# Kernel tuning notes

Measured on AMD Instinct MI355X. Metric: run time of the kernel, lower is better.

Reference implementation:

```python
import jax, jax.numpy as jnp
import numpy as np

B, S, D = 4, 2048, 1024
E, H, K = 32, 128, 2


def setup_inputs() -> dict:
    key = jax.random.key(0)
    k1, k2, k3, k4 = jax.random.split(key, 4)
    scale_d = 1.0 / np.sqrt(D)
    scale_h = 1.0 / np.sqrt(H)
    return {
        "x": jax.random.normal(k1, (B, S, D), dtype=jnp.float32),
        "w_sel": jax.random.normal(k2, (E, D), dtype=jnp.float32) * scale_d,      # router Linear weight [E, D]
        "w_keys": jax.random.normal(k3, (E, D, H), dtype=jnp.float32) * scale_d,  # per-expert up-proj
        "w_values": jax.random.normal(k4, (E, H, D), dtype=jnp.float32) * scale_h, # per-expert down-proj
        "k": K,
    }


def reference(x, w_sel, w_keys, w_values, k):
    # Router: sigmoid gating + top-k expert selection per token.
    sel = jax.nn.sigmoid(jnp.einsum('bsd,ed->bse', x, w_sel))      # [B,S,E]
    sel_val, sel_idx = jax.lax.top_k(sel, k)                       # [B,S,k]
    n_exp = w_sel.shape[0]
    # Dense gate matrix: gate[b,s,e] = sum of sel_val over heads routed to e
    # (top_k indices are distinct, so this matches the per-head accumulation).
    gate = jnp.sum(jax.nn.one_hot(sel_idx, n_exp, dtype=x.dtype) * sel_val[..., None], axis=-2)  # [B,S,E]
    # Expert up-projection + ReLU for all experts (dense equivalent of the
    # per-token gathered keys[expert_idx](token); unselected experts are
    # zeroed by the gate so the math is identical).
    scores = jax.nn.relu(jnp.einsum('bsd,edh->bseh', x, w_keys))   # [B,S,E,H]
    weighted = scores * gate[..., None]                            # [B,S,E,H]
    out = jnp.einsum('bseh,ehd->bsd', weighted, w_values)          # [B,S,D]
    return out
```

## Files before the change

kernel.cpp:

```cpp
#include <hip/hip_runtime.h>
#include <cstdint>
#include <cstddef>

#define NTOK 8192
#define DIM  1024
#define NEXP 32
#define NH   128
#define TT   64
#define FTILES 16
#define BK   128
#define RT   32
#define LCAP 1024

typedef __attribute__((ext_vector_type(8))) short short8;
typedef __attribute__((ext_vector_type(4))) float float4_;

static __device__ __forceinline__ unsigned short f2bf(float f) {
  unsigned u = __float_as_uint(f);
  return (unsigned short)((u + 0x7fffu + ((u >> 16) & 1u)) >> 16);
}
static __device__ __forceinline__ float bf2f(unsigned short h) {
  return __uint_as_float(((unsigned)h) << 16);
}
static __device__ __forceinline__ void gload_lds16(const unsigned short* g,
                                                   unsigned short* l) {
  __builtin_amdgcn_global_load_lds(
      (const __attribute__((address_space(1))) unsigned int*)(const void*)g,
      (__attribute__((address_space(3))) unsigned int*)(void*)l, 16, 0, 0);
}

__global__ __launch_bounds__(256) void prep_kernel(
    const float* __restrict__ w_keys, const float* __restrict__ w_values,
    const float* __restrict__ x,
    unsigned short* __restrict__ wk_t, unsigned short* __restrict__ wv_t,
    unsigned short* __restrict__ xbf, int* __restrict__ counts)
{
  __shared__ float tile[32][33];
  const int bid = blockIdx.x;
  const int tid = threadIdx.x;
  if (bid == 0 && tid < NEXP) counts[tid] = 0;

  if (bid < 8192) {
    const float* src; unsigned short* dst; int R, C, lb;
    if (bid < 4096) { src = w_keys;   dst = wk_t; R = DIM; C = NH;  lb = bid; }
    else            { src = w_values; dst = wv_t; R = NH;  C = DIM; lb = bid - 4096; }
    const int e  = lb >> 7;
    const int t  = lb & 127;
    const int tpc = C >> 5;
    const int r0 = (t / tpc) * 32;
    const int c0 = (t % tpc) * 32;
    const float* s = src + (size_t)e * R * C;
    unsigned short* d = dst + (size_t)e * R * C;

    const int i = tid >> 3;
    const int j = (tid & 7) * 4;
    float4 v = *(const float4*)(s + (size_t)(r0 + i) * C + c0 + j);
    tile[i][j] = v.x; tile[i][j + 1] = v.y; tile[i][j + 2] = v.z; tile[i][j + 3] = v.w;
    __syncthreads();
    unsigned lo = (unsigned)f2bf(tile[j + 0][i]) | ((unsigned)f2bf(tile[j + 1][i]) << 16);
    unsigned hi = (unsigned)f2bf(tile[j + 2][i]) | ((unsigned)f2bf(tile[j + 3][i]) << 16);
    uint2 u; u.x = lo; u.y = hi;
    *(uint2*)(d + (size_t)(c0 + i) * R + r0 + j) = u;
  } else {
    const int lb = bid - 8192;
    size_t i = ((size_t)lb * 256 + tid) * 8;
    float4 a = *(const float4*)(x + i);
    float4 b = *(const float4*)(x + i + 4);
    uint4 u;
    u.x = (unsigned)f2bf(a.x) | ((unsigned)f2bf(a.y) << 16);
    u.y = (unsigned)f2bf(a.z) | ((unsigned)f2bf(a.w) << 16);
    u.z = (unsigned)f2bf(b.x) | ((unsigned)f2bf(b.y) << 16);
    u.w = (unsigned)f2bf(b.z) | ((unsigned)f2bf(b.w) << 16);
    *(uint4*)(xbf + i) = u;
  }
}

__global__ __launch_bounds__(256) void router_kernel(
    const float* __restrict__ x, const float* __restrict__ w_sel,
    int* __restrict__ counts, unsigned* __restrict__ list)
{
  __shared__ __align__(16) float xs_t[64][36];
  __shared__ float ws[NEXP][65];
  __shared__ float S[RT][33];

  const int tid  = threadIdx.x;
  const int tok0 = blockIdx.x * RT;
  const int tr   = tid >> 3;
  const int d8   = (tid & 7) * 8;
  const int tg4  = (tid & 7) * 4;

  float acc[4] = {0.f, 0.f, 0.f, 0.f};

  for (int dc = 0; dc < DIM; dc += 64) {
    const float* xp = x + (size_t)(tok0 + tr) * DIM + dc + d8;
    float4 a0 = *(const float4*)(xp);
    float4 a1 = *(const float4*)(xp + 4);
    xs_t[d8 + 0][tr] = a0.x; xs_t[d8 + 1][tr] = a0.y;
    xs_t[d8 + 2][tr] = a0.z; xs_t[d8 + 3][tr] = a0.w;
    xs_t[d8 + 4][tr] = a1.x; xs_t[d8 + 5][tr] = a1.y;
    xs_t[d8 + 6][tr] = a1.z; xs_t[d8 + 7][tr] = a1.w;
    const float* wp = w_sel + (size_t)tr * DIM + dc + d8;
    float4 b0 = *(const float4*)(wp);
    float4 b1 = *(const float4*)(wp + 4);
    ws[tr][d8 + 0] = b0.x; ws[tr][d8 + 1] = b0.y;
    ws[tr][d8 + 2] = b0.z; ws[tr][d8 + 3] = b0.w;
    ws[tr][d8 + 4] = b1.x; ws[tr][d8 + 5] = b1.y;
    ws[tr][d8 + 6] = b1.z; ws[tr][d8 + 7] = b1.w;
    __syncthreads();

    #pragma unroll 8
    for (int d = 0; d < 64; ++d) {
      float w = ws[tr][d];
      float4 xv = *(const float4*)&xs_t[d][tg4];
      acc[0] += xv.x * w; acc[1] += xv.y * w;
      acc[2] += xv.z * w; acc[3] += xv.w * w;
    }
    __syncthreads();
  }

  #pragma unroll
  for (int j = 0; j < 4; ++j)
    S[tg4 + j][tr] = acc[j];
  __syncthreads();

  if (tid < RT) {
    const int t = tid;
    float m1 = -1e30f, m2 = -1e30f;
    int i1 = 0, i2 = 0;
    for (int ee = 0; ee < NEXP; ++ee) {
      float v = S[t][ee];
      if (v > m1)      { m2 = m1; i2 = i1; m1 = v; i1 = ee; }
      else if (v > m2) { m2 = v; i2 = ee; }
    }
    const int token = tok0 + t;
    float g1 = 1.f / (1.f + __expf(-m1));
    float g2 = 1.f / (1.f + __expf(-m2));
    unsigned e1 = ((unsigned)f2bf(g1) << 16) | ((unsigned)token << 1);
    unsigned e2 = ((unsigned)f2bf(g2) << 16) | ((unsigned)token << 1) | 1u;
    int p1 = atomicAdd(&counts[i1], 1);
    if (p1 < LCAP) list[i1 * LCAP + p1] = e1;
    int p2 = atomicAdd(&counts[i2], 1);
    if (p2 < LCAP) list[i2 * LCAP + p2] = e2;
  }
}

__global__ __launch_bounds__(256, 2) void ffn_kernel(
    const unsigned short* __restrict__ xbf,
    const unsigned short* __restrict__ wk_t,
    const unsigned short* __restrict__ wv_t,
    float* __restrict__ out,
    unsigned short* __restrict__ cont,
    const int* __restrict__ counts, const unsigned* __restrict__ list,
    int use_cont)
{
  const int bid = blockIdx.x;
  const int e   = bid & 31;
  const int cnt = min(counts[e], LCAP);

  __shared__ unsigned short xsf[2][16 * 512];
  __shared__ unsigned short ss[TT][NH + 8];
  __shared__ int   toks[TT];
  __shared__ float gates[TT];

  const int tid  = threadIdx.x;
  const int wave = tid >> 6;
  const int lane = tid & 63;
  const int quad = lane >> 4;
  const int l16  = lane & 15;

  const unsigned short* wkb = wk_t + (size_t)e * NH * DIM;
  const unsigned short* wvb = wv_t + (size_t)e * DIM * NH;

  for (int t0 = (bid >> 5) * TT; t0 < cnt; t0 += FTILES * TT) {
    const int n_tok = min(TT, cnt - t0);

    if (tid < TT) {
      int valid = tid < n_tok;
      unsigned en = valid ? list[e * LCAP + t0 + tid] : 0u;
      toks[tid]  = valid ? (int)(en & 0xffffu) : -1;
      gates[tid] = valid ? bf2f((unsigned short)(en >> 16)) : 0.f;
    }
    __syncthreads();

    int slot = toks[wave * 16 + l16];
    int gtok = (slot < 0) ? 0 : (slot >> 1);
    const unsigned short* gsrc = xbf + (size_t)gtok * DIM + quad * 8;

    #pragma unroll
    for (int kk = 0; kk < 4; ++kk)
      gload_lds16(gsrc + kk * 32, &xsf[0][(wave * 4 + kk) * 512]);
    __syncthreads();

    float4_ acc[4][2];
    #pragma unroll
    for (int mt = 0; mt < 4; ++mt)
      #pragma unroll
      for (int nt = 0; nt < 2; ++nt) acc[mt][nt] = (float4_){0.f, 0.f, 0.f, 0.f};

    for (int ci = 0; ci < 8; ++ci) {
      const int dc = ci * BK;
      if (ci < 7) {
        const int nb = (ci + 1) & 1;
        #pragma unroll
        for (int kk = 0; kk < 4; ++kk)
          gload_lds16(gsrc + dc + BK + kk * 32, &xsf[nb][(wave * 4 + kk) * 512]);
      }
      short8 b[4][2];
      #pragma unroll
      for (int kk = 0; kk < 4; ++kk)
        #pragma unroll
        for (int nt = 0; nt < 2; ++nt)
          b[kk][nt] = *(const short8*)(wkb +
              (size_t)(wave * 32 + nt * 16 + l16) * DIM + dc + kk * 32 + quad * 8);

      const unsigned short* xb = &xsf[ci & 1][0];
      #pragma unroll
      for (int kk = 0; kk < 4; ++kk) {
        #pragma unroll
        for (int mt = 0; mt < 4; ++mt) {
          short8 a = *(const short8*)(xb + (mt * 4 + kk) * 512 + lane * 8);
          #pragma unroll
          for (int nt = 0; nt < 2; ++nt)
            acc[mt][nt] = __builtin_amdgcn_mfma_f32_16x16x32_bf16(a, b[kk][nt], acc[mt][nt], 0, 0, 0);
        }
      }
      __syncthreads();
    }

    #pragma unroll
    for (int mt = 0; mt < 4; ++mt)
      #pragma unroll
      for (int nt = 0; nt < 2; ++nt)
        #pragma unroll
        for (int r = 0; r < 4; ++r) {
          int row = mt * 16 + quad * 4 + r;
          float v = fmaxf(acc[mt][nt][r], 0.f) * gates[row];
          ss[row][wave * 32 + nt * 16 + l16] = f2bf(v);
        }
    __syncthreads();

    #pragma unroll 1
    for (int nc = 0; nc < 4; ++nc) {
      const int colbase = wave * 256 + nc * 64;
      float4_ o[4][4];
      #pragma unroll
      for (int mt = 0; mt < 4; ++mt)
        #pragma unroll
        for (int nt = 0; nt < 4; ++nt) o[mt][nt] = (float4_){0.f, 0.f, 0.f, 0.f};

      short8 b2[4][4];
      #pragma unroll
      for (int kk = 0; kk < 4; ++kk)
        #pragma unroll
        for (int nt = 0; nt < 4; ++nt)
          b2[kk][nt] = *(const short8*)(wvb +
              (size_t)(colbase + nt * 16 + l16) * NH + kk * 32 + quad * 8);

      #pragma unroll
      for (int kk = 0; kk < 4; ++kk) {
        short8 a[4];
        #pragma unroll
        for (int mt = 0; mt < 4; ++mt)
          a[mt] = *(const short8*)&ss[mt * 16 + l16][kk * 32 + quad * 8];
        #pragma unroll
        for (int mt = 0; mt < 4; ++mt)
          #pragma unroll
          for (int nt = 0; nt < 4; ++nt)
            o[mt][nt] = __builtin_amdgcn_mfma_f32_16x16x32_bf16(a[mt], b2[kk][nt], o[mt][nt], 0, 0, 0);
      }

      if (use_cont) {
        #pragma unroll
        for (int mt = 0; mt < 4; ++mt)
          #pragma unroll
          for (int r = 0; r < 4; ++r) {
            int row = mt * 16 + quad * 4 + r;
            if (row < n_tok) {
              int sl = toks[row];
              size_t base = ((size_t)((sl & 1) * NTOK + (sl >> 1))) * DIM + colbase;
              #pragma unroll
              for (int nt = 0; nt < 4; ++nt)
                cont[base + nt * 16 + l16] = f2bf(o[mt][nt][r]);
            }
          }
      } else {
        #pragma unroll
        for (int mt = 0; mt < 4; ++mt)
          #pragma unroll
          for (int r = 0; r < 4; ++r) {
            int row = mt * 16 + quad * 4 + r;
            if (row < n_tok) {
              size_t base = (size_t)(toks[row] >> 1) * DIM + colbase;
              #pragma unroll
              for (int nt = 0; nt < 4; ++nt)
                unsafeAtomicAdd(&out[base + nt * 16 + l16], o[mt][nt][r]);
            }
          }
      }
    }
    __syncthreads();
  }
}

__global__ __launch_bounds__(256) void combine_kernel(
    const unsigned short* __restrict__ cont, float* __restrict__ out)
{
  size_t i = ((size_t)blockIdx.x * 256 + threadIdx.x) * 8;
  uint4 a = *(const uint4*)(cont + i);
  uint4 b = *(const uint4*)(cont + (size_t)NTOK * DIM + i);
  float4 r0, r1;
  r0.x = bf2f((unsigned short)(a.x & 0xffff)) + bf2f((unsigned short)(b.x & 0xffff));
  r0.y = bf2f((unsigned short)(a.x >> 16))    + bf2f((unsigned short)(b.x >> 16));
  r0.z = bf2f((unsigned short)(a.y & 0xffff)) + bf2f((unsigned short)(b.y & 0xffff));
  r0.w = bf2f((unsigned short)(a.y >> 16))    + bf2f((unsigned short)(b.y >> 16));
  r1.x = bf2f((unsigned short)(a.z & 0xffff)) + bf2f((unsigned short)(b.z & 0xffff));
  r1.y = bf2f((unsigned short)(a.z >> 16))    + bf2f((unsigned short)(b.z >> 16));
  r1.z = bf2f((unsigned short)(a.w & 0xffff)) + bf2f((unsigned short)(b.w & 0xffff));
  r1.w = bf2f((unsigned short)(a.w >> 16))    + bf2f((unsigned short)(b.w >> 16));
  *(float4*)(out + i) = r0;
  *(float4*)(out + i + 4) = r1;
}

extern "C" void kernel_launch(void* const* d_in, const int* in_sizes, int n_in,
                              void* d_out, int out_size, void* d_ws, size_t ws_size,
                              hipStream_t stream) {
  (void)in_sizes; (void)n_in;
  const float* x        = (const float*)d_in[0];
  const float* w_sel    = (const float*)d_in[1];
  const float* w_keys   = (const float*)d_in[2];
  const float* w_values = (const float*)d_in[3];
  float* out = (float*)d_out;

  char* ws = (char*)d_ws;
  size_t off = 0;
  int*            counts = (int*)(ws + off);            off += 4096;
  unsigned*       list   = (unsigned*)(ws + off);       off += (size_t)NEXP * LCAP * 4;
  unsigned short* wk_t   = (unsigned short*)(ws + off); off += (size_t)NEXP * NH * DIM * 2;
  unsigned short* wv_t   = (unsigned short*)(ws + off); off += (size_t)NEXP * NH * DIM * 2;
  unsigned short* xbf    = (unsigned short*)(ws + off); off += (size_t)NTOK * DIM * 2;
  unsigned short* cont   = (unsigned short*)(ws + off);
  size_t need_full = off + (size_t)2 * NTOK * DIM * 2;
  const int use_cont = (ws_size >= need_full) ? 1 : 0;

  prep_kernel<<<12288, 256, 0, stream>>>(w_keys, w_values, x, wk_t, wv_t, xbf, counts);

  router_kernel<<<NTOK / RT, 256, 0, stream>>>(x, w_sel, counts, list);

  if (!use_cont)
    hipMemsetAsync(out, 0, (size_t)out_size * sizeof(float), stream);

  ffn_kernel<<<NEXP * FTILES, 256, 0, stream>>>(xbf, wk_t, wv_t, out, cont,
                                                counts, list, use_cont);

  if (use_cont)
    combine_kernel<<<NTOK * DIM / (256 * 8), 256, 0, stream>>>(cont, out);
}
```

Measured before the change: 249.8 us.

## Fuse x bf16 conversion into FFN, split routing lists per choice, flatten tile grid

The FFN kernel now reads fp32 x directly and converts it to bf16 while staging each tile, so the separate x conversion pass and its bf16 buffer go away. Routing lists are kept per (expert, choice), and blocks are mapped onto a flattened tile list rather than a fixed per-expert grid. First-choice results are written in fp32 straight to the output, and second-choice results go to a bf16 buffer, so the combine kernel reads a single bf16 buffer and adds it into the output. The router is rewritten as direct per-thread dot products without LDS tiling, the FFN prefetches weights into registers, and the counts are cleared with a small memset. The fixed grid of 320 blocks and a per-list cap of 512 can silently drop tokens if routing is very skewed.

```diff
diff --git a/kernel.cpp b/kernel.cpp
--- a/kernel.cpp
+++ b/kernel.cpp
@@ -1,4 +1,5 @@
 #include <hip/hip_runtime.h>
+#include <hip/hip_bf16.h>
 #include <cstdint>
 #include <cstddef>
 
@@ -7,10 +8,10 @@
 #define NEXP 32
 #define NH   128
 #define TT   64
-#define FTILES 16
 #define BK   128
-#define RT   32
-#define LCAP 1024
+#define LCAP2 512
+#define RTOK 16
+#define FGRID 320
 
 typedef __attribute__((ext_vector_type(8))) short short8;
 typedef __attribute__((ext_vector_type(4))) float float4_;
@@ -22,283 +23,296 @@
 static __device__ __forceinline__ float bf2f(unsigned short h) {
   return __uint_as_float(((unsigned)h) << 16);
 }
-static __device__ __forceinline__ void gload_lds16(const unsigned short* g,
-                                                   unsigned short* l) {
-  __builtin_amdgcn_global_load_lds(
-      (const __attribute__((address_space(1))) unsigned int*)(const void*)g,
-      (__attribute__((address_space(3))) unsigned int*)(void*)l, 16, 0, 0);
-}
-
-__global__ __launch_bounds__(256) void prep_kernel(
+
+__global__ __launch_bounds__(256) void transpose_cvt_kernel(
     const float* __restrict__ w_keys, const float* __restrict__ w_values,
-    const float* __restrict__ x,
-    unsigned short* __restrict__ wk_t, unsigned short* __restrict__ wv_t,
-    unsigned short* __restrict__ xbf, int* __restrict__ counts)
+    unsigned short* __restrict__ wk_t, unsigned short* __restrict__ wv_t)
 {
   __shared__ float tile[32][33];
   const int bid = blockIdx.x;
   const int tid = threadIdx.x;
-  if (bid == 0 && tid < NEXP) counts[tid] = 0;
-
-  if (bid < 8192) {
-    const float* src; unsigned short* dst; int R, C, lb;
-    if (bid < 4096) { src = w_keys;   dst = wk_t; R = DIM; C = NH;  lb = bid; }
-    else            { src = w_values; dst = wv_t; R = NH;  C = DIM; lb = bid - 4096; }
-    const int e  = lb >> 7;
-    const int t  = lb & 127;
-    const int tpc = C >> 5;
-    const int r0 = (t / tpc) * 32;
-    const int c0 = (t % tpc) * 32;
-    const float* s = src + (size_t)e * R * C;
-    unsigned short* d = dst + (size_t)e * R * C;
-
-    const int i = tid >> 3;
-    const int j = (tid & 7) * 4;
-    float4 v = *(const float4*)(s + (size_t)(r0 + i) * C + c0 + j);
-    tile[i][j] = v.x; tile[i][j + 1] = v.y; tile[i][j + 2] = v.z; tile[i][j + 3] = v.w;
-    __syncthreads();
-    unsigned lo = (unsigned)f2bf(tile[j + 0][i]) | ((unsigned)f2bf(tile[j + 1][i]) << 16);
-    unsigned hi = (unsigned)f2bf(tile[j + 2][i]) | ((unsigned)f2bf(tile[j + 3][i]) << 16);
-    uint2 u; u.x = lo; u.y = hi;
-    *(uint2*)(d + (size_t)(c0 + i) * R + r0 + j) = u;
-  } else {
-    const int lb = bid - 8192;
-    size_t i = ((size_t)lb * 256 + tid) * 8;
-    float4 a = *(const float4*)(x + i);
-    float4 b = *(const float4*)(x + i + 4);
-    uint4 u;
-    u.x = (unsigned)f2bf(a.x) | ((unsigned)f2bf(a.y) << 16);
-    u.y = (unsigned)f2bf(a.z) | ((unsigned)f2bf(a.w) << 16);
-    u.z = (unsigned)f2bf(b.x) | ((unsigned)f2bf(b.y) << 16);
-    u.w = (unsigned)f2bf(b.z) | ((unsigned)f2bf(b.w) << 16);
-    *(uint4*)(xbf + i) = u;
-  }
+  const float* src; unsigned short* dst; int R, C, lb;
+  if (bid < 4096) { src = w_keys;   dst = wk_t; R = DIM; C = NH;  lb = bid; }
+  else            { src = w_values; dst = wv_t; R = NH;  C = DIM; lb = bid - 4096; }
+  const int e   = lb >> 7;
+  const int t   = lb & 127;
+  const int tpc = C >> 5;
+  const int r0  = (t / tpc) * 32;
+  const int c0  = (t % tpc) * 32;
+  const float* s = src + (size_t)e * R * C;
+  unsigned short* d = dst + (size_t)e * R * C;
+
+  const int i = tid >> 3;
+  const int j = (tid & 7) * 4;
+  float4 v = *(const float4*)(s + (size_t)(r0 + i) * C + c0 + j);
+  tile[i][j] = v.x; tile[i][j + 1] = v.y; tile[i][j + 2] = v.z; tile[i][j + 3] = v.w;
+  __syncthreads();
+  unsigned lo = (unsigned)f2bf(tile[j + 0][i]) | ((unsigned)f2bf(tile[j + 1][i]) << 16);
+  unsigned hi = (unsigned)f2bf(tile[j + 2][i]) | ((unsigned)f2bf(tile[j + 3][i]) << 16);
+  uint2 u; u.x = lo; u.y = hi;
+  *(uint2*)(d + (size_t)(c0 + i) * R + r0 + j) = u;
 }
 
 __global__ __launch_bounds__(256) void router_kernel(
     const float* __restrict__ x, const float* __restrict__ w_sel,
     int* __restrict__ counts, unsigned* __restrict__ list)
 {
-  __shared__ __align__(16) float xs_t[64][36];
-  __shared__ float ws[NEXP][65];
-  __shared__ float S[RT][33];
-
+  __shared__ float sp[RTOK][33];
   const int tid  = threadIdx.x;
-  const int tok0 = blockIdx.x * RT;
-  const int tr   = tid >> 3;
-  const int d8   = (tid & 7) * 8;
-  const int tg4  = (tid & 7) * 4;
-
-  float acc[4] = {0.f, 0.f, 0.f, 0.f};
-
-  for (int dc = 0; dc < DIM; dc += 64) {
-    const float* xp = x + (size_t)(tok0 + tr) * DIM + dc + d8;
-    float4 a0 = *(const float4*)(xp);
-    float4 a1 = *(const float4*)(xp + 4);
-    xs_t[d8 + 0][tr] = a0.x; xs_t[d8 + 1][tr] = a0.y;
-    xs_t[d8 + 2][tr] = a0.z; xs_t[d8 + 3][tr] = a0.w;
-    xs_t[d8 + 4][tr] = a1.x; xs_t[d8 + 5][tr] = a1.y;
-    xs_t[d8 + 6][tr] = a1.z; xs_t[d8 + 7][tr] = a1.w;
-    const float* wp = w_sel + (size_t)tr * DIM + dc + d8;
-    float4 b0 = *(const float4*)(wp);
-    float4 b1 = *(const float4*)(wp + 4);
-    ws[tr][d8 + 0] = b0.x; ws[tr][d8 + 1] = b0.y;
-    ws[tr][d8 + 2] = b0.z; ws[tr][d8 + 3] = b0.w;
-    ws[tr][d8 + 4] = b1.x; ws[tr][d8 + 5] = b1.y;
-    ws[tr][d8 + 6] = b1.z; ws[tr][d8 + 7] = b1.w;
-    __syncthreads();
-
-    #pragma unroll 8
-    for (int d = 0; d < 64; ++d) {
-      float w = ws[tr][d];
-      float4 xv = *(const float4*)&xs_t[d][tg4];
-      acc[0] += xv.x * w; acc[1] += xv.y * w;
-      acc[2] += xv.z * w; acc[3] += xv.w * w;
-    }
-    __syncthreads();
-  }
-
-  #pragma unroll
-  for (int j = 0; j < 4; ++j)
-    S[tg4 + j][tr] = acc[j];
-  __syncthreads();
-
-  if (tid < RT) {
+  const int tok0 = blockIdx.x * RTOK;
+  const int e    = tid & 31;
+  const int tq   = tid >> 5;
+
+  const float* xr = x + (size_t)(tok0 + tq * 2) * DIM;
+  const float* wr = w_sel + (size_t)e * DIM;
+
+  float acc0 = 0.f, acc1 = 0.f;
+
+  #pragma unroll 2
+  for (int dc = 0; dc < DIM; dc += 16) {
+    float4 w0 = *(const float4*)(wr + dc + 0);
+    float4 w1 = *(const float4*)(wr + dc + 4);
+    float4 w2 = *(const float4*)(wr + dc + 8);
+    float4 w3 = *(const float4*)(wr + dc + 12);
+    float4 xa0 = *(const float4*)(xr + dc + 0);
+    float4 xa1 = *(const float4*)(xr + dc + 4);
+    float4 xa2 = *(const float4*)(xr + dc + 8);
+    float4 xa3 = *(const float4*)(xr + dc + 12);
+    float4 xb0 = *(const float4*)(xr + DIM + dc + 0);
+    float4 xb1 = *(const float4*)(xr + DIM + dc + 4);
+    float4 xb2 = *(const float4*)(xr + DIM + dc + 8);
+    float4 xb3 = *(const float4*)(xr + DIM + dc + 12);
+    acc0 += xa0.x*w0.x + xa0.y*w0.y + xa0.z*w0.z + xa0.w*w0.w
+          + xa1.x*w1.x + xa1.y*w1.y + xa1.z*w1.z + xa1.w*w1.w
+          + xa2.x*w2.x + xa2.y*w2.y + xa2.z*w2.z + xa2.w*w2.w
+          + xa3.x*w3.x + xa3.y*w3.y + xa3.z*w3.z + xa3.w*w3.w;
+    acc1 += xb0.x*w0.x + xb0.y*w0.y + xb0.z*w0.z + xb0.w*w0.w
+          + xb1.x*w1.x + xb1.y*w1.y + xb1.z*w1.z + xb1.w*w1.w
+          + xb2.x*w2.x + xb2.y*w2.y + xb2.z*w2.z + xb2.w*w2.w
+          + xb3.x*w3.x + xb3.y*w3.y + xb3.z*w3.z + xb3.w*w3.w;
+  }
+
+  sp[tq * 2 + 0][e] = acc0;
+  sp[tq * 2 + 1][e] = acc1;
+  __syncthreads();
+
+  if (tid < RTOK) {
     const int t = tid;
     float m1 = -1e30f, m2 = -1e30f;
     int i1 = 0, i2 = 0;
     for (int ee = 0; ee < NEXP; ++ee) {
-      float v = S[t][ee];
+      float v = sp[t][ee];
       if (v > m1)      { m2 = m1; i2 = i1; m1 = v; i1 = ee; }
       else if (v > m2) { m2 = v; i2 = ee; }
     }
     const int token = tok0 + t;
     float g1 = 1.f / (1.f + __expf(-m1));
     float g2 = 1.f / (1.f + __expf(-m2));
-    unsigned e1 = ((unsigned)f2bf(g1) << 16) | ((unsigned)token << 1);
-    unsigned e2 = ((unsigned)f2bf(g2) << 16) | ((unsigned)token << 1) | 1u;
-    int p1 = atomicAdd(&counts[i1], 1);
-    if (p1 < LCAP) list[i1 * LCAP + p1] = e1;
-    int p2 = atomicAdd(&counts[i2], 1);
-    if (p2 < LCAP) list[i2 * LCAP + p2] = e2;
-  }
-}
-
-__global__ __launch_bounds__(256, 2) void ffn_kernel(
-    const unsigned short* __restrict__ xbf,
+    int p1 = atomicAdd(&counts[i1 * 2 + 0], 1);
+    if (p1 < LCAP2) list[(i1 * 2 + 0) * LCAP2 + p1] = ((unsigned)f2bf(g1) << 16) | (unsigned)token;
+    int p2 = atomicAdd(&counts[i2 * 2 + 1], 1);
+    if (p2 < LCAP2) list[(i2 * 2 + 1) * LCAP2 + p2] = ((unsigned)f2bf(g2) << 16) | (unsigned)token;
+  }
+}
+
+__global__ __launch_bounds__(256, 1) void ffn_kernel(
+    const float* __restrict__ x,
     const unsigned short* __restrict__ wk_t,
     const unsigned short* __restrict__ wv_t,
     float* __restrict__ out,
     unsigned short* __restrict__ cont,
-    const int* __restrict__ counts, const unsigned* __restrict__ list,
-    int use_cont)
+    const int* __restrict__ counts, const unsigned* __restrict__ list)
 {
-  const int bid = blockIdx.x;
-  const int e   = bid & 31;
-  const int cnt = min(counts[e], LCAP);
-
-  __shared__ unsigned short xsf[2][16 * 512];
-  __shared__ unsigned short ss[TT][NH + 8];
+  __shared__ __align__(16) unsigned short xs[2][TT][BK + 8];
+  __shared__ __align__(16) unsigned short ss[TT][NH + 8];
+  __shared__ int   cnts_s[64];
   __shared__ int   toks[TT];
   __shared__ float gates[TT];
 
-  const int tid  = threadIdx.x;
+  const int tid = threadIdx.x;
+  if (tid < 64) cnts_s[tid] = min(counts[tid], LCAP2);
+  __syncthreads();
+
+  int tile = blockIdx.x;
+  int ec = -1, cnt = 0;
+  for (int i = 0; i < 64; ++i) {
+    int c  = cnts_s[i];
+    int nt = (c + TT - 1) >> 6;
+    if (ec < 0) {
+      if (tile < nt) { ec = i; cnt = c; }
+      else tile -= nt;
+    }
+  }
+  if (ec < 0) return;
+  const int e      = ec >> 1;
+  const int choice = ec & 1;
+  const int t0     = tile * TT;
+  const int n_tok  = min(TT, cnt - t0);
+
+  const unsigned* lst = list + (size_t)ec * LCAP2;
+  if (tid < TT) {
+    int valid = tid < n_tok;
+    unsigned en = valid ? lst[t0 + tid] : 0u;
+    toks[tid]  = (int)(en & 0xffffu);
+    gates[tid] = valid ? bf2f((unsigned short)(en >> 16)) : 0.f;
+  }
+  __syncthreads();
+
   const int wave = tid >> 6;
   const int lane = tid & 63;
   const int quad = lane >> 4;
   const int l16  = lane & 15;
+  const int st   = tid >> 2;
+  const int sd   = (tid & 3) * 32;
 
   const unsigned short* wkb = wk_t + (size_t)e * NH * DIM;
   const unsigned short* wvb = wv_t + (size_t)e * DIM * NH;
-
-  for (int t0 = (bid >> 5) * TT; t0 < cnt; t0 += FTILES * TT) {
-    const int n_tok = min(TT, cnt - t0);
-
-    if (tid < TT) {
-      int valid = tid < n_tok;
-      unsigned en = valid ? list[e * LCAP + t0 + tid] : 0u;
-      toks[tid]  = valid ? (int)(en & 0xffffu) : -1;
-      gates[tid] = valid ? bf2f((unsigned short)(en >> 16)) : 0.f;
+  const float* xrow = x + (size_t)toks[st] * DIM + sd;
+
+  {
+    float4 f[8];
+    #pragma unroll
+    for (int q = 0; q < 8; ++q) f[q] = *(const float4*)(xrow + q * 4);
+    #pragma unroll
+    for (int p = 0; p < 4; ++p) {
+      union { short8 s; __hip_bfloat162 h[4]; } u;
+      u.h[0] = __float22bfloat162_rn(float2{f[2*p].x,   f[2*p].y});
+      u.h[1] = __float22bfloat162_rn(float2{f[2*p].z,   f[2*p].w});
+      u.h[2] = __float22bfloat162_rn(float2{f[2*p+1].x, f[2*p+1].y});
+      u.h[3] = __float22bfloat162_rn(float2{f[2*p+1].z, f[2*p+1].w});
+      *(short8*)&xs[0][st][sd + p * 8] = u.s;
+    }
+  }
+  __syncthreads();
+
+  float4_ acc[4][2];
+  #pragma unroll
+  for (int mt = 0; mt < 4; ++mt)
+    #pragma unroll
+    for (int nt = 0; nt < 2; ++nt) acc[mt][nt] = (float4_){0.f, 0.f, 0.f, 0.f};
+
+  short8 bA[2][4][2];
+  #pragma unroll
+  for (int kk = 0; kk < 4; ++kk)
+    #pragma unroll
+    for (int nt = 0; nt < 2; ++nt)
+      bA[0][kk][nt] = *(const short8*)(wkb +
+          (size_t)(wave * 32 + nt * 16 + l16) * DIM + kk * 32 + quad * 8);
+
+  float4 xf[8];
+  #pragma unroll
+  for (int ci = 0; ci < 8; ++ci) {
+    const int cur = ci & 1;
+    if (ci < 7) {
+      #pragma unroll
+      for (int q = 0; q < 8; ++q)
+        xf[q] = *(const float4*)(xrow + (ci + 1) * BK + q * 4);
+    }
+    if (ci < 7) {
+      #pragma unroll
+      for (int kk = 0; kk < 4; ++kk)
+        #pragma unroll
+        for (int nt = 0; nt < 2; ++nt)
+          bA[cur ^ 1][kk][nt] = *(const short8*)(wkb +
+              (size_t)(wave * 32 + nt * 16 + l16) * DIM + (ci + 1) * BK + kk * 32 + quad * 8);
+    }
+    #pragma unroll
+    for (int kk = 0; kk < 4; ++kk) {
+      short8 a[4];
+      #pragma unroll
+      for (int mt = 0; mt < 4; ++mt)
+        a[mt] = *(const short8*)&xs[cur][mt * 16 + l16][kk * 32 + quad * 8];
+      #pragma unroll
+      for (int mt = 0; mt < 4; ++mt)
+        #pragma unroll
+        for (int nt = 0; nt < 2; ++nt)
+          acc[mt][nt] = __builtin_amdgcn_mfma_f32_16x16x32_bf16(a[mt], bA[cur][kk][nt], acc[mt][nt], 0, 0, 0);
+    }
+    if (ci < 7) {
+      #pragma unroll
+      for (int p = 0; p < 4; ++p) {
+        union { short8 s; __hip_bfloat162 h[4]; } u;
+        u.h[0] = __float22bfloat162_rn(float2{xf[2*p].x,   xf[2*p].y});
+        u.h[1] = __float22bfloat162_rn(float2{xf[2*p].z,   xf[2*p].w});
+        u.h[2] = __float22bfloat162_rn(float2{xf[2*p+1].x, xf[2*p+1].y});
+        u.h[3] = __float22bfloat162_rn(float2{xf[2*p+1].z, xf[2*p+1].w});
+        *(short8*)&xs[cur ^ 1][st][sd + p * 8] = u.s;
+      }
     }
     __syncthreads();
-
-    int slot = toks[wave * 16 + l16];
-    int gtok = (slot < 0) ? 0 : (slot >> 1);
-    const unsigned short* gsrc = xbf + (size_t)gtok * DIM + quad * 8;
-
+  }
+
+  #pragma unroll
+  for (int mt = 0; mt < 4; ++mt)
+    #pragma unroll
+    for (int nt = 0; nt < 2; ++nt)
+      #pragma unroll
+      for (int r = 0; r < 4; ++r) {
+        int row = mt * 16 + quad * 4 + r;
+        float v = fmaxf(acc[mt][nt][r], 0.f) * gates[row];
+        ss[row][wave * 32 + nt * 16 + l16] = f2bf(v);
+      }
+  __syncthreads();
+
+  short8 a2[4][4];
+  #pragma unroll
+  for (int mt = 0; mt < 4; ++mt)
     #pragma unroll
     for (int kk = 0; kk < 4; ++kk)
-      gload_lds16(gsrc + kk * 32, &xsf[0][(wave * 4 + kk) * 512]);
-    __syncthreads();
-
-    float4_ acc[4][2];
+      a2[mt][kk] = *(const short8*)&ss[mt * 16 + l16][kk * 32 + quad * 8];
+
+  #pragma unroll
+  for (int nc = 0; nc < 4; ++nc) {
+    const int colbase = wave * 256 + nc * 64;
+    short8 b2[4][4];
+    #pragma unroll
+    for (int kk = 0; kk < 4; ++kk)
+      #pragma unroll
+      for (int nt = 0; nt < 4; ++nt)
+        b2[kk][nt] = *(const short8*)(wvb +
+            (size_t)(colbase + nt * 16 + l16) * NH + kk * 32 + quad * 8);
+
+    float4_ o[4][4];
     #pragma unroll
     for (int mt = 0; mt < 4; ++mt)
       #pragma unroll
-      for (int nt = 0; nt < 2; ++nt) acc[mt][nt] = (float4_){0.f, 0.f, 0.f, 0.f};
-
-    for (int ci = 0; ci < 8; ++ci) {
-      const int dc = ci * BK;
-      if (ci < 7) {
-        const int nb = (ci + 1) & 1;
-        #pragma unroll
-        for (int kk = 0; kk < 4; ++kk)
-          gload_lds16(gsrc + dc + BK + kk * 32, &xsf[nb][(wave * 4 + kk) * 512]);
-      }
-      short8 b[4][2];
-      #pragma unroll
-      for (int kk = 0; kk < 4; ++kk)
-        #pragma unroll
-        for (int nt = 0; nt < 2; ++nt)
-          b[kk][nt] = *(const short8*)(wkb +
-              (size_t)(wave * 32 + nt * 16 + l16) * DIM + dc + kk * 32 + quad * 8);
-
-      const unsigned short* xb = &xsf[ci & 1][0];
-      #pragma unroll
-      for (int kk = 0; kk < 4; ++kk) {
-        #pragma unroll
-        for (int mt = 0; mt < 4; ++mt) {
-          short8 a = *(const short8*)(xb + (mt * 4 + kk) * 512 + lane * 8);
-          #pragma unroll
-          for (int nt = 0; nt < 2; ++nt)
-            acc[mt][nt] = __builtin_amdgcn_mfma_f32_16x16x32_bf16(a, b[kk][nt], acc[mt][nt], 0, 0, 0);
-        }
-      }
-      __syncthreads();
-    }
-
-    #pragma unroll
-    for (int mt = 0; mt < 4; ++mt)
-      #pragma unroll
-      for (int nt = 0; nt < 2; ++nt)
+      for (int nt = 0; nt < 4; ++nt) o[mt][nt] = (float4_){0.f, 0.f, 0.f, 0.f};
+
+    #pragma unroll
+    for (int kk = 0; kk < 4; ++kk)
+      #pragma unroll
+      for (int mt = 0; mt < 4; ++mt)
+        #pragma unroll
+        for (int nt = 0; nt < 4; ++nt)
+          o[mt][nt] = __builtin_amdgcn_mfma_f32_16x16x32_bf16(a2[mt][kk], b2[kk][nt], o[mt][nt], 0, 0, 0);
+
+    if (choice == 0) {
+      #pragma unroll
+      for (int mt = 0; mt < 4; ++mt)
         #pragma unroll
         for (int r = 0; r < 4; ++r) {
           int row = mt * 16 + quad * 4 + r;
-          float v = fmaxf(acc[mt][nt][r], 0.f) * gates[row];
-          ss[row][wave * 32 + nt * 16 + l16] = f2bf(v);
+          if (row < n_tok) {
+            float* basep = out + (size_t)toks[row] * DIM + colbase + l16;
+            #pragma unroll
+            for (int nt = 0; nt < 4; ++nt)
+              basep[nt * 16] = o[mt][nt][r];
+          }
         }
-    __syncthreads();
-
-    #pragma unroll 1
-    for (int nc = 0; nc < 4; ++nc) {
-      const int colbase = wave * 256 + nc * 64;
-      float4_ o[4][4];
-      #pragma unroll
-      for (int mt = 0; mt < 4; ++mt)
-        #pragma unroll
-        for (int nt = 0; nt < 4; ++nt) o[mt][nt] = (float4_){0.f, 0.f, 0.f, 0.f};
-
-      short8 b2[4][4];
-      #pragma unroll
-      for (int kk = 0; kk < 4; ++kk)
-        #pragma unroll
-        for (int nt = 0; nt < 4; ++nt)
-          b2[kk][nt] = *(const short8*)(wvb +
-              (size_t)(colbase + nt * 16 + l16) * NH + kk * 32 + quad * 8);
-
-      #pragma unroll
-      for (int kk = 0; kk < 4; ++kk) {
-        short8 a[4];
-        #pragma unroll
-        for (int mt = 0; mt < 4; ++mt)
-          a[mt] = *(const short8*)&ss[mt * 16 + l16][kk * 32 + quad * 8];
-        #pragma unroll
-        for (int mt = 0; mt < 4; ++mt)
-          #pragma unroll
-          for (int nt = 0; nt < 4; ++nt)
-            o[mt][nt] = __builtin_amdgcn_mfma_f32_16x16x32_bf16(a[mt], b2[kk][nt], o[mt][nt], 0, 0, 0);
-      }
-
-      if (use_cont) {
-        #pragma unroll
-        for (int mt = 0; mt < 4; ++mt)
-          #pragma unroll
-          for (int r = 0; r < 4; ++r) {
-            int row = mt * 16 + quad * 4 + r;
-            if (row < n_tok) {
-              int sl = toks[row];
-              size_t base = ((size_t)((sl & 1) * NTOK + (sl >> 1))) * DIM + colbase;
-              #pragma unroll
-              for (int nt = 0; nt < 4; ++nt)
-                cont[base + nt * 16 + l16] = f2bf(o[mt][nt][r]);
-            }
+    } else {
+      #pragma unroll
+      for (int mt = 0; mt < 4; ++mt)
+        #pragma unroll
+        for (int r = 0; r < 4; ++r) {
+          int row = mt * 16 + quad * 4 + r;
+          if (row < n_tok) {
+            unsigned short* basep = cont + (size_t)toks[row] * DIM + colbase + l16;
+            #pragma unroll
+            for (int nt = 0; nt < 4; ++nt)
+              basep[nt * 16] = f2bf(o[mt][nt][r]);
           }
-      } else {
-        #pragma unroll
-        for (int mt = 0; mt < 4; ++mt)
-          #pragma unroll
-          for (int r = 0; r < 4; ++r) {
-            int row = mt * 16 + quad * 4 + r;
-            if (row < n_tok) {
-              size_t base = (size_t)(toks[row] >> 1) * DIM + colbase;
-              #pragma unroll
-              for (int nt = 0; nt < 4; ++nt)
-                unsafeAtomicAdd(&out[base + nt * 16 + l16], o[mt][nt][r]);
-            }
-          }
-      }
-    }
-    __syncthreads();
+        }
+    }
   }
 }
 
@@ -306,25 +320,25 @@
     const unsigned short* __restrict__ cont, float* __restrict__ out)
 {
   size_t i = ((size_t)blockIdx.x * 256 + threadIdx.x) * 8;
-  uint4 a = *(const uint4*)(cont + i);
-  uint4 b = *(const uint4*)(cont + (size_t)NTOK * DIM + i);
-  float4 r0, r1;
-  r0.x = bf2f((unsigned short)(a.x & 0xffff)) + bf2f((unsigned short)(b.x & 0xffff));
-  r0.y = bf2f((unsigned short)(a.x >> 16))    + bf2f((unsigned short)(b.x >> 16));
-  r0.z = bf2f((unsigned short)(a.y & 0xffff)) + bf2f((unsigned short)(b.y & 0xffff));
-  r0.w = bf2f((unsigned short)(a.y >> 16))    + bf2f((unsigned short)(b.y >> 16));
-  r1.x = bf2f((unsigned short)(a.z & 0xffff)) + bf2f((unsigned short)(b.z & 0xffff));
-  r1.y = bf2f((unsigned short)(a.z >> 16))    + bf2f((unsigned short)(b.z >> 16));
-  r1.z = bf2f((unsigned short)(a.w & 0xffff)) + bf2f((unsigned short)(b.w & 0xffff));
-  r1.w = bf2f((unsigned short)(a.w >> 16))    + bf2f((unsigned short)(b.w >> 16));
-  *(float4*)(out + i) = r0;
-  *(float4*)(out + i + 4) = r1;
+  uint4 c = *(const uint4*)(cont + i);
+  float4 o0 = *(const float4*)(out + i);
+  float4 o1 = *(const float4*)(out + i + 4);
+  o0.x += bf2f((unsigned short)(c.x & 0xffff));
+  o0.y += bf2f((unsigned short)(c.x >> 16));
+  o0.z += bf2f((unsigned short)(c.y & 0xffff));
+  o0.w += bf2f((unsigned short)(c.y >> 16));
+  o1.x += bf2f((unsigned short)(c.z & 0xffff));
+  o1.y += bf2f((unsigned short)(c.z >> 16));
+  o1.z += bf2f((unsigned short)(c.w & 0xffff));
+  o1.w += bf2f((unsigned short)(c.w >> 16));
+  *(float4*)(out + i)     = o0;
+  *(float4*)(out + i + 4) = o1;
 }
 
 extern "C" void kernel_launch(void* const* d_in, const int* in_sizes, int n_in,
                               void* d_out, int out_size, void* d_ws, size_t ws_size,
                               hipStream_t stream) {
-  (void)in_sizes; (void)n_in;
+  (void)in_sizes; (void)n_in; (void)ws_size; (void)out_size;
   const float* x        = (const float*)d_in[0];
   const float* w_sel    = (const float*)d_in[1];
   const float* w_keys   = (const float*)d_in[2];
@@ -334,24 +348,18 @@
   char* ws = (char*)d_ws;
   size_t off = 0;
   int*            counts = (int*)(ws + off);            off += 4096;
-  unsigned*       list   = (unsigned*)(ws + off);       off += (size_t)NEXP * LCAP * 4;
+  unsigned*       list   = (unsigned*)(ws + off);       off += (size_t)NEXP * 2 * LCAP2 * 4;
   unsigned short* wk_t   = (unsigned short*)(ws + off); off += (size_t)NEXP * NH * DIM * 2;
   unsigned short* wv_t   = (unsigned short*)(ws + off); off += (size_t)NEXP * NH * DIM * 2;
-  unsigned short* xbf    = (unsigned short*)(ws + off); off += (size_t)NTOK * DIM * 2;
   unsigned short* cont   = (unsigned short*)(ws + off);
-  size_t need_full = off + (size_t)2 * NTOK * DIM * 2;
-  const int use_cont = (ws_size >= need_full) ? 1 : 0;
-
-  prep_kernel<<<12288, 256, 0, stream>>>(w_keys, w_values, x, wk_t, wv_t, xbf, counts);
-
-  router_kernel<<<NTOK / RT, 256, 0, stream>>>(x, w_sel, counts, list);
-
-  if (!use_cont)
-    hipMemsetAsync(out, 0, (size_t)out_size * sizeof(float), stream);
-
-  ffn_kernel<<<NEXP * FTILES, 256, 0, stream>>>(xbf, wk_t, wv_t, out, cont,
-                                                counts, list, use_cont);
-
-  if (use_cont)
-    combine_kernel<<<NTOK * DIM / (256 * 8), 256, 0, stream>>>(cont, out);
-}
+
+  hipMemsetAsync(counts, 0, sizeof(int) * NEXP * 2, stream);
+
+  transpose_cvt_kernel<<<8192, 256, 0, stream>>>(w_keys, w_values, wk_t, wv_t);
+
+  router_kernel<<<NTOK / RTOK, 256, 0, stream>>>(x, w_sel, counts, list);
+
+  ffn_kernel<<<FGRID, 256, 0, stream>>>(x, wk_t, wv_t, out, cont, counts, list);
+
+  combine_kernel<<<NTOK * DIM / (256 * 8), 256, 0, stream>>>(cont, out);
+}
```

Result: slower. 288.7 us (+15.6%).
